# Performance work log

Hardware: AMD Instinct MI355X
Metric: run time of the kernel (lower is better)

Reference implementation:

```python
import jax, jax.numpy as jnp
import numpy as np

H = 8
D_MODEL = 1024
DIM_G = 64
WAVE_LEN = 1000.0


def box_relational_embedding(f_g):
    # f_g: [B, N, 4] -> [B, N, N, 64] trigonometric geometry embedding
    B, N, _ = f_g.shape
    x_min, y_min, x_max, y_max = jnp.split(f_g, 4, axis=-1)  # each [B, N, 1]
    cx = (x_min + x_max) * 0.5
    cy = (y_min + y_max) * 0.5
    w = x_max - x_min + 1.0
    h = y_max - y_min + 1.0
    # row i vs column j deltas, normalized by row box size
    dx = jnp.log(jnp.maximum(jnp.abs((cx - cx.reshape(B, 1, N)) / w), 1e-3))
    dy = jnp.log(jnp.maximum(jnp.abs((cy - cy.reshape(B, 1, N)) / h), 1e-3))
    dw = jnp.log(w / w.reshape(B, 1, N))
    dh = jnp.log(h / h.reshape(B, 1, N))
    pos = jnp.stack([dx, dy, dw, dh], axis=-1)  # [B, N, N, 4]
    feat_range = jnp.arange(DIM_G // 8, dtype=jnp.float32) / (DIM_G / 8.0)
    dim_mat = 1.0 / jnp.power(WAVE_LEN, feat_range)  # [8]
    mul = (100.0 * pos)[..., None] * dim_mat  # [B, N, N, 4, 8]
    mul = mul.reshape(B, N, N, DIM_G // 2)
    return jnp.concatenate([jnp.sin(mul), jnp.cos(mul)], axis=-1)  # [B, N, N, 64]


def setup_inputs() -> dict:
    key = jax.random.key(0)
    ks = jax.random.split(key, 12)
    B, N, D = 16, 256, D_MODEL
    q = jax.random.normal(ks[0], (B, N, D), jnp.float32)
    k = jax.random.normal(ks[1], (B, N, D), jnp.float32)
    v = jax.random.normal(ks[2], (B, N, D), jnp.float32)
    # valid boxes: x_max > x_min, y_max > y_min
    xy = jax.random.uniform(ks[3], (B, N, 2), jnp.float32) * 100.0
    wh = jax.random.uniform(ks[4], (B, N, 2), jnp.float32) * 50.0 + 1.0
    input_box = jnp.concatenate([xy, xy + wh], axis=-1)  # [B, N, 4]
    s = 0.02
    Wq = jax.random.normal(ks[5], (D, D), jnp.float32) * s
    Wk = jax.random.normal(ks[6], (D, D), jnp.float32) * s
    Wv = jax.random.normal(ks[7], (D, D), jnp.float32) * s
    Wo = jax.random.normal(ks[8], (D, D), jnp.float32) * s
    bq = jnp.zeros((D,), jnp.float32)
    bk = jnp.zeros((D,), jnp.float32)
    bv = jnp.zeros((D,), jnp.float32)
    bo = jnp.zeros((D,), jnp.float32)
    Wg = jax.random.normal(ks[9], (H, DIM_G), jnp.float32) * 0.1  # stacked per-head Linear(64,1)
    bg = jax.random.normal(ks[10], (H,), jnp.float32) * 0.1
    return {"input_query": q, "input_key": k, "input_value": v, "input_box": input_box,
            "Wq": Wq, "bq": bq, "Wk": Wk, "bk": bk, "Wv": Wv, "bv": bv,
            "Wg": Wg, "bg": bg, "Wo": Wo, "bo": bo}


def reference(input_query, input_key, input_value, input_box,
              Wq, bq, Wk, bk, Wv, bv, Wg, bg, Wo, bo):
    B, N, D = input_query.shape
    d_k = D // H

    def proj(x, W, b):
        return (x @ W + b).reshape(B, N, H, d_k).transpose(0, 2, 1, 3)  # [B,H,N,dk]

    q = proj(input_query, Wq, bq)
    k = proj(input_key, Wk, bk)
    v = proj(input_value, Wv, bv)

    emb = box_relational_embedding(input_box)  # [B, N, N, 64]
    # per-head Linear(64 -> 1), stacked: [B, H, N, N]
    rel_w = jax.nn.relu(jnp.einsum('bmng,hg->bhmn', emb, Wg) + bg[None, :, None, None])

    scores = jnp.einsum('bhqd,bhkd->bhqk', q, k) / np.sqrt(d_k).astype(np.float32)
    logits = jnp.log(jnp.maximum(rel_w, 1e-6)) + scores
    attn = jax.nn.softmax(logits, axis=-1)  # [B, H, N, N]
    out = jnp.einsum('bhqk,bhkd->bhqd', attn, v)
    out = out.transpose(0, 2, 1, 3).reshape(B, N, D)
    return out @ Wo + bo
```

## Files before the change

### kernel.cpp

```cpp
#include <hip/hip_runtime.h>
#include <hip/hip_bf16.h>
#include <hip/hip_fp16.h>
#include <math.h>

#define B_  16
#define N_  256
#define D_  1024
#define H_  8
#define DK_ 128

typedef unsigned short u16;
typedef __attribute__((ext_vector_type(8))) short s8v;
typedef __attribute__((ext_vector_type(4))) float f4v;

__device__ __forceinline__ u16 f2b(float x) {
    union { float f; unsigned u; } v; v.f = x;
    unsigned r = v.u + 0x7fffu + ((v.u >> 16) & 1u);
    return (u16)(r >> 16);
}

__device__ __forceinline__ void gload16(void* lds, const void* g) {
    __builtin_amdgcn_global_load_lds(
        (const __attribute__((address_space(1))) void*)g,
        (__attribute__((address_space(3))) void*)lds, 16, 0, 0);
}

#define WV_(n) asm volatile("s_waitcnt vmcnt(" #n ")" ::: "memory")
#define WV(n)  WV_(n)
#define MEMBAR() asm volatile("" ::: "memory")

__global__ __launch_bounds__(256)
void cvt_kernel(const float* __restrict__ x0, const float* __restrict__ x1,
                const float* __restrict__ x2, u16* __restrict__ out)
{
    const float* in = (blockIdx.y == 0) ? x0 : (blockIdx.y == 1) ? x1 : x2;
    u16* o = out + (size_t)blockIdx.y * 4194304;
    const int i = blockIdx.x * 256 + threadIdx.x;
    const float4 a = ((const float4*)in)[2 * i];
    const float4 b = ((const float4*)in)[2 * i + 1];
    union { u16 s[8]; uint4 v; } t;
    t.s[0] = f2b(a.x); t.s[1] = f2b(a.y); t.s[2] = f2b(a.z); t.s[3] = f2b(a.w);
    t.s[4] = f2b(b.x); t.s[5] = f2b(b.y); t.s[6] = f2b(b.z); t.s[7] = f2b(b.w);
    ((uint4*)o)[i] = t.v;
}

__global__ __launch_bounds__(256)
void cvtT_kernel(const float* __restrict__ W0, const float* __restrict__ W1,
                 const float* __restrict__ W2, const float* __restrict__ W3,
                 u16* __restrict__ out)
{
    const float* W = (blockIdx.z == 0) ? W0 : (blockIdx.z == 1) ? W1 :
                     (blockIdx.z == 2) ? W2 : W3;
    u16* o = out + (size_t)blockIdx.z * (D_ * D_);
    __shared__ float t[32][33];
    const int k0 = blockIdx.x * 32, n0 = blockIdx.y * 32;
    const int c = threadIdx.x & 31, r8 = threadIdx.x >> 5;
#pragma unroll
    for (int rr = 0; rr < 4; ++rr)
        t[r8 + rr * 8][c] = W[(size_t)(k0 + r8 + rr * 8) * D_ + n0 + c];
    __syncthreads();
#pragma unroll
    for (int rr = 0; rr < 4; ++rr)
        o[(size_t)(n0 + r8 + rr * 8) * D_ + k0 + c] = f2b(t[c][r8 + rr * 8]);
}

#define AOFF(s,mh) (((s)*2+(mh))*8192)
#define BOFF(s,nh) (32768 + ((s)*2+(nh))*8192)

#define STG_A(ns, mh, kn) do { \
    gload16(&lds8[AOFF(ns,mh) + adst],        aS + (size_t)(m0 + (mh)*64) * 1024 + (kn)); \
    gload16(&lds8[AOFF(ns,mh) + 4096 + adst], aS + (size_t)(m0 + 128 + (mh)*64) * 1024 + (kn)); \
} while (0)

#define STG_B(ns, nh, kn) do { \
    gload16(&lds8[BOFF(ns,nh) + bdst],        bS + (size_t)(n0 + (nh)*32) * 1024 + (kn)); \
    gload16(&lds8[BOFF(ns,nh) + 4096 + bdst], bS + (size_t)(n0 + 128 + (nh)*32) * 1024 + (kn)); \
} while (0)

#define TILE(S, W0, W1, W2, DOSTG, KN) do { \
     \
    WV(W0); __builtin_amdgcn_s_barrier(); \
    _Pragma("unroll") \
    for (int i = 0; i < 4; ++i) { \
        af[i][0] = *(const s8v*)&lds8[AOFF(S,0) + ar + i * 1024 + o0]; \
        af[i][1] = *(const s8v*)&lds8[AOFF(S,0) + ar + i * 1024 + o1]; } \
    _Pragma("unroll") \
    for (int j = 0; j < 2; ++j) { \
        bf0[j][0] = *(const s8v*)&lds8[BOFF(S,0) + br + j * 1024 + o0]; \
        bf0[j][1] = *(const s8v*)&lds8[BOFF(S,0) + br + j * 1024 + o1]; } \
    if (DOSTG) { STG_A((S)^1, 0, KN); STG_B((S)^1, 0, KN); } \
    __builtin_amdgcn_s_setprio(1); \
    _Pragma("unroll") \
    for (int i = 0; i < 4; ++i) \
        _Pragma("unroll") \
        for (int j = 0; j < 2; ++j) { \
            acc[i][j] = __builtin_amdgcn_mfma_f32_16x16x32_bf16(af[i][0], bf0[j][0], acc[i][j], 0, 0, 0); \
            acc[i][j] = __builtin_amdgcn_mfma_f32_16x16x32_bf16(af[i][1], bf0[j][1], acc[i][j], 0, 0, 0); } \
    __builtin_amdgcn_s_setprio(0); \
     \
    WV(W1); __builtin_amdgcn_s_barrier(); \
    _Pragma("unroll") \
    for (int j = 0; j < 2; ++j) { \
        bf1[j][0] = *(const s8v*)&lds8[BOFF(S,1) + br + j * 1024 + o0]; \
        bf1[j][1] = *(const s8v*)&lds8[BOFF(S,1) + br + j * 1024 + o1]; } \
    if (DOSTG) { STG_B((S)^1, 1, KN); } \
    __builtin_amdgcn_s_setprio(1); \
    _Pragma("unroll") \
    for (int i = 0; i < 4; ++i) \
        _Pragma("unroll") \
        for (int j = 0; j < 2; ++j) { \
            acc[i][2+j] = __builtin_amdgcn_mfma_f32_16x16x32_bf16(af[i][0], bf1[j][0], acc[i][2+j], 0, 0, 0); \
            acc[i][2+j] = __builtin_amdgcn_mfma_f32_16x16x32_bf16(af[i][1], bf1[j][1], acc[i][2+j], 0, 0, 0); } \
    __builtin_amdgcn_s_setprio(0); \
     \
    WV(W2); __builtin_amdgcn_s_barrier(); \
    _Pragma("unroll") \
    for (int i = 0; i < 4; ++i) { \
        af[i][0] = *(const s8v*)&lds8[AOFF(S,1) + ar + i * 1024 + o0]; \
        af[i][1] = *(const s8v*)&lds8[AOFF(S,1) + ar + i * 1024 + o1]; } \
    if (DOSTG) { STG_A((S)^1, 1, KN); } \
    __builtin_amdgcn_s_setprio(1); \
    _Pragma("unroll") \
    for (int i = 0; i < 4; ++i) \
        _Pragma("unroll") \
        for (int j = 0; j < 2; ++j) { \
            acc[4+i][2+j] = __builtin_amdgcn_mfma_f32_16x16x32_bf16(af[i][0], bf1[j][0], acc[4+i][2+j], 0, 0, 0); \
            acc[4+i][2+j] = __builtin_amdgcn_mfma_f32_16x16x32_bf16(af[i][1], bf1[j][1], acc[4+i][2+j], 0, 0, 0); } \
    __builtin_amdgcn_s_setprio(0); \
     \
    __builtin_amdgcn_s_setprio(1); \
    _Pragma("unroll") \
    for (int i = 0; i < 4; ++i) \
        _Pragma("unroll") \
        for (int j = 0; j < 2; ++j) { \
            acc[4+i][j] = __builtin_amdgcn_mfma_f32_16x16x32_bf16(af[i][0], bf0[j][0], acc[4+i][j], 0, 0, 0); \
            acc[4+i][j] = __builtin_amdgcn_mfma_f32_16x16x32_bf16(af[i][1], bf0[j][1], acc[4+i][j], 0, 0, 0); } \
    __builtin_amdgcn_s_setprio(0); \
} while (0)

template<int MODE>
__global__ __launch_bounds__(512, 2)
void gemm8(const u16* __restrict__ A0, const u16* __restrict__ Wt0,
           const float* __restrict__ b0, const float* __restrict__ b1,
           const float* __restrict__ b2, void* __restrict__ outb)
{
    extern __shared__ u16 lds8[];

    const int z = blockIdx.z;
    const u16* A  = A0  + (size_t)z * 4194304;
    const u16* Wt = Wt0 + (size_t)z * 1048576;
    const float* bias = (z == 0) ? b0 : (z == 1) ? b1 : b2;

    const int bid = blockIdx.x;
    const int m0  = (bid & 15) * 256;
    const int n0  = (bid >> 4) * 256;

    const int tid  = threadIdx.x;
    const int lane = tid & 63;
    const int w    = tid >> 6;
    const int l15  = lane & 15;
    const int l4   = lane >> 4;
    const int wr   = w >> 2;
    const int wc   = w & 3;

    const int ar = wr * 4096 + l15 * 64;
    const int br = wc * 2048 + l15 * 64;
    const int o0 = (l4 ^ (l15 & 7)) * 8;
    const int o1 = o0 ^ 32;

    const int rA   = tid >> 3;
    const int cswz = ((tid & 7) ^ (rA & 7)) * 8;
    const u16* aS  = A  + (size_t)rA * 1024 + cswz;
    const u16* bS  = Wt + (size_t)((tid >> 8) * 64 + (rA & 31)) * 1024 + cswz;
    const int adst = rA * 64 + (tid & 7) * 8;
    const int bdst = (tid >> 8) * 2048 + (rA & 31) * 64 + (tid & 7) * 8;

    f4v acc[8][4] = {};
    s8v af[4][2], bf0[2][2], bf1[2][2];

    STG_A(0, 0, 0); STG_B(0, 0, 0); MEMBAR();
    STG_B(0, 1, 0); MEMBAR();
    STG_A(0, 1, 0); MEMBAR();

#pragma unroll 1
    for (int tt = 0; tt < 14; tt += 2) {
        TILE(0, 4, 6, 6, true, (tt + 1) * 64);
        TILE(1, 4, 6, 6, true, (tt + 2) * 64);
    }
    TILE(0, 4, 6, 6, true, 15 * 64);
    TILE(1, 4, 2, 0, false, 0);

#pragma unroll
    for (int mh = 0; mh < 2; ++mh)
#pragma unroll
    for (int i = 0; i < 4; ++i)
#pragma unroll
    for (int nh = 0; nh < 2; ++nh)
#pragma unroll
    for (int j = 0; j < 2; ++j) {
        const int n = n0 + wc * 64 + nh * 32 + j * 16 + l15;
        const float bb = bias[n];
        const int mbase = m0 + wr * 128 + mh * 64 + i * 16 + l4 * 4;
        const f4v a = acc[mh * 4 + i][nh * 2 + j];
        if constexpr (MODE == 0) {
#pragma unroll
            for (int reg = 0; reg < 4; ++reg)
                ((float*)outb)[(size_t)(mbase + reg) * 1024 + n] = a[reg] + bb;
        } else {
            if (z == 2) {
                const int b = mbase >> 8, tok = mbase & 255;
                const int h = n >> 7, d = n & 127;
                ushort4 st;
                st.x = f2b(a[0] + bb); st.y = f2b(a[1] + bb);
                st.z = f2b(a[2] + bb); st.w = f2b(a[3] + bb);
                *(ushort4*)&((u16*)outb)[(size_t)z * 4194304 +
                    (((size_t)b * H_ + h) * DK_ + d) * N_ + tok] = st;
            } else {
                const int h = n >> 7, d = n & 127;
#pragma unroll
                for (int reg = 0; reg < 4; ++reg) {
                    const int m = mbase + reg;
                    const int b = m >> 8, tok = m & 255;
                    ((u16*)outb)[(size_t)z * 4194304 +
                        (((size_t)b * H_ + h) * N_ + tok) * DK_ + d] = f2b(a[reg] + bb);
                }
            }
        }
    }
}

__global__ __launch_bounds__(256)
void boxbias_kernel(const float* __restrict__ fg, const float* __restrict__ Wg,
                    const float* __restrict__ bg, _Float16* __restrict__ lb)
{
    __shared__ float sWg[512];
    __shared__ float sbg[8];
    const int tid = threadIdx.x;
    const int b = blockIdx.x >> 8;
    const int i = blockIdx.x & 255;

    sWg[tid] = Wg[tid];
    sWg[tid + 256] = Wg[tid + 256];
    if (tid < 8) sbg[tid] = bg[tid];

    const float4 bi = *(const float4*)&fg[(size_t)(b * N_ + i) * 4];
    const float cxi = 0.5f * (bi.x + bi.z);
    const float cyi = 0.5f * (bi.y + bi.w);
    const float wi  = bi.z - bi.x + 1.0f;
    const float hi  = bi.w - bi.y + 1.0f;

    const int j = tid;
    const float4 bj = *(const float4*)&fg[(size_t)(b * N_ + j) * 4];
    const float cxj = 0.5f * (bj.x + bj.z);
    const float cyj = 0.5f * (bj.y + bj.w);
    const float wj  = bj.z - bj.x + 1.0f;
    const float hj  = bj.w - bj.y + 1.0f;

    const float pos[4] = {
        logf(fmaxf(fabsf((cxi - cxj) / wi), 1e-3f)) * 100.0f,
        logf(fmaxf(fabsf((cyi - cyj) / hi), 1e-3f)) * 100.0f,
        logf(wi / wj) * 100.0f,
        logf(hi / hj) * 100.0f
    };
    const float dim[8] = {1.0f, 0.421696503f, 0.177827941f, 0.0749894209f,
                          0.0316227766f, 0.0133352143f, 0.00562341325f, 0.00237137371f};

    float sv[32], cv[32];
#pragma unroll
    for (int p = 0; p < 4; ++p)
#pragma unroll
        for (int q = 0; q < 8; ++q)
            __sincosf(pos[p] * dim[q], &sv[p * 8 + q], &cv[p * 8 + q]);

    __syncthreads();
#pragma unroll
    for (int h = 0; h < 8; ++h) {
        float acc = sbg[h];
        const float* wrow = &sWg[h * 64];
#pragma unroll
        for (int g = 0; g < 32; ++g)
            acc = fmaf(sv[g], wrow[g], fmaf(cv[g], wrow[32 + g], acc));
        const float rel = fmaxf(acc, 0.0f);
        lb[(((size_t)b * H_ + h) * N_ + i) * N_ + j] =
            (_Float16)logf(fmaxf(rel, 1e-6f));
    }
}

__global__ __launch_bounds__(256)
void attn_mfma_kernel(const u16* __restrict__ qp, const u16* __restrict__ kp,
                      const u16* __restrict__ vp, const _Float16* __restrict__ lb,
                      u16* __restrict__ ao)
{
    __shared__ __align__(16) u16 Ks[32][136];
    __shared__ __align__(16) u16 Vt[128][40];
    __shared__ __align__(16) u16 Ps[4][32][40];

    const int tid  = threadIdx.x;
    const int lane = tid & 63;
    const int w    = tid >> 6;
    const int l15  = lane & 15;
    const int l4   = lane >> 4;
    const int bh   = blockIdx.x >> 1;
    const int qt   = blockIdx.x & 1;
    const int q0   = qt * 128 + w * 32;

    s8v qf[2][4];
    const u16* qb = qp + ((size_t)bh * N_ + q0) * DK_;
#pragma unroll
    for (int mf = 0; mf < 2; ++mf)
#pragma unroll
        for (int ks = 0; ks < 4; ++ks)
            qf[mf][ks] = *(const s8v*)(qb + (size_t)(mf * 16 + l15) * DK_ + ks * 32 + l4 * 8);

    f4v o[2][8] = {};
    float m_r[2][4], l_r[2][4];
#pragma unroll
    for (int mf = 0; mf < 2; ++mf)
#pragma unroll
        for (int r = 0; r < 4; ++r) { m_r[mf][r] = -INFINITY; l_r[mf][r] = 0.0f; }

    const float scale = 0.08838834764831845f;
    const _Float16* lbb = lb + ((size_t)bh * N_ + q0) * N_;

    const int sr = tid >> 3;
    const int sc = (tid & 7) * 16;
    const int vr = tid >> 2;
    const int vs = (tid & 3) * 8;

    for (int kt = 0; kt < 8; ++kt) {
        __syncthreads();
        {
            const u16* ksrc = kp + ((size_t)bh * N_ + kt * 32) * DK_;
            *(s8v*)&Ks[sr][sc]     = *(const s8v*)(ksrc + (size_t)sr * DK_ + sc);
            *(s8v*)&Ks[sr][sc + 8] = *(const s8v*)(ksrc + (size_t)sr * DK_ + sc + 8);
        }
        {
            const u16* vsrc = vp + ((size_t)bh * DK_ + vr) * N_ + kt * 32 + vs;
            const s8v v0 = *(const s8v*)vsrc;
            const s8v v1 = *(const s8v*)(vsrc + 64 * N_);
            *(s8v*)&Vt[vr][vs]      = v0;
            *(s8v*)&Vt[vr + 64][vs] = v1;
        }
        __syncthreads();

        f4v s[2][2] = {};
#pragma unroll
        for (int ks = 0; ks < 4; ++ks) {
#pragma unroll
            for (int kf = 0; kf < 2; ++kf) {
                const s8v kb = *(const s8v*)&Ks[kf * 16 + l15][ks * 32 + l4 * 8];
#pragma unroll
                for (int mf = 0; mf < 2; ++mf)
                    s[mf][kf] = __builtin_amdgcn_mfma_f32_16x16x32_bf16(
                        qf[mf][ks], kb, s[mf][kf], 0, 0, 0);
            }
        }
#pragma unroll
        for (int mf = 0; mf < 2; ++mf)
#pragma unroll
            for (int kf = 0; kf < 2; ++kf)
#pragma unroll
                for (int r = 0; r < 4; ++r)
                    s[mf][kf][r] = fmaf(s[mf][kf][r], scale, (float)
                        lbb[(size_t)(mf * 16 + l4 * 4 + r) * N_ + kt * 32 + kf * 16 + l15]);

#pragma unroll
        for (int mf = 0; mf < 2; ++mf) {
            float rm[4], al[4];
#pragma unroll
            for (int r = 0; r < 4; ++r) rm[r] = fmaxf(s[mf][0][r], s[mf][1][r]);
#pragma unroll
            for (int st = 1; st <= 8; st <<= 1)
#pragma unroll
                for (int r = 0; r < 4; ++r) rm[r] = fmaxf(rm[r], __shfl_xor(rm[r], st));
#pragma unroll
            for (int r = 0; r < 4; ++r) {
                const float mn = fmaxf(m_r[mf][r], rm[r]);
                al[r] = __expf(m_r[mf][r] - mn);
                m_r[mf][r] = mn;
            }
            float p0[4], p1[4], rs[4];
#pragma unroll
            for (int r = 0; r < 4; ++r) {
                p0[r] = __expf(s[mf][0][r] - m_r[mf][r]);
                p1[r] = __expf(s[mf][1][r] - m_r[mf][r]);
                rs[r] = p0[r] + p1[r];
            }
#pragma unroll
            for (int st = 1; st <= 8; st <<= 1)
#pragma unroll
                for (int r = 0; r < 4; ++r) rs[r] += __shfl_xor(rs[r], st);
#pragma unroll
            for (int r = 0; r < 4; ++r) {
                l_r[mf][r] = l_r[mf][r] * al[r] + rs[r];
                Ps[w][mf * 16 + l4 * 4 + r][l15]      = f2b(p0[r]);
                Ps[w][mf * 16 + l4 * 4 + r][16 + l15] = f2b(p1[r]);
            }
#pragma unroll
            for (int nf = 0; nf < 8; ++nf)
#pragma unroll
                for (int r = 0; r < 4; ++r) o[mf][nf][r] *= al[r];
        }

        s8v pa[2];
#pragma unroll
        for (int mf = 0; mf < 2; ++mf)
            pa[mf] = *(const s8v*)&Ps[w][mf * 16 + l15][l4 * 8];
#pragma unroll
        for (int nf = 0; nf < 8; ++nf) {
            const s8v vb = *(const s8v*)&Vt[nf * 16 + l15][l4 * 8];
#pragma unroll
            for (int mf = 0; mf < 2; ++mf)
                o[mf][nf] = __builtin_amdgcn_mfma_f32_16x16x32_bf16(
                    pa[mf], vb, o[mf][nf], 0, 0, 0);
        }
    }

    const int b = bh >> 3, h = bh & 7;
#pragma unroll
    for (int mf = 0; mf < 2; ++mf) {
        float inv[4];
#pragma unroll
        for (int r = 0; r < 4; ++r) inv[r] = 1.0f / l_r[mf][r];
#pragma unroll
        for (int nf = 0; nf < 8; ++nf) {
#pragma unroll
            for (int r = 0; r < 4; ++r) {
                const int tok = q0 + mf * 16 + l4 * 4 + r;
                const int d = nf * 16 + l15;
                ao[(((size_t)b * N_ + tok) * H_ + h) * DK_ + d] = f2b(o[mf][nf][r] * inv[r]);
            }
        }
    }
}

extern "C" void kernel_launch(void* const* d_in, const int* in_sizes, int n_in,
                              void* d_out, int out_size, void* d_ws, size_t ws_size,
                              hipStream_t stream)
{
    const float* xq = (const float*)d_in[0];
    const float* xk = (const float*)d_in[1];
    const float* xv = (const float*)d_in[2];
    const float* fg = (const float*)d_in[3];
    const float* Wq = (const float*)d_in[4];
    const float* bq = (const float*)d_in[5];
    const float* Wk = (const float*)d_in[6];
    const float* bk = (const float*)d_in[7];
    const float* Wv = (const float*)d_in[8];
    const float* bv = (const float*)d_in[9];
    const float* Wg = (const float*)d_in[10];
    const float* bg = (const float*)d_in[11];
    const float* Wo = (const float*)d_in[12];
    const float* bo = (const float*)d_in[13];

    char* w8 = (char*)d_ws;
    u16*      xb  = (u16*)(w8);
    u16*      Wt  = (u16*)(w8 + 25165824);
    u16*      qkv = (u16*)(w8 + 33554432);
    _Float16* lb  = (_Float16*)(w8 + 58720256);
    u16*      ao  = (u16*)(w8 + 75497472);

    (void)hipFuncSetAttribute(reinterpret_cast<const void*>(&gemm8<1>),
                              hipFuncAttributeMaxDynamicSharedMemorySize, 131072);
    (void)hipFuncSetAttribute(reinterpret_cast<const void*>(&gemm8<0>),
                              hipFuncAttributeMaxDynamicSharedMemorySize, 131072);

    cvt_kernel<<<dim3(2048, 3), 256, 0, stream>>>(xq, xk, xv, xb);
    cvtT_kernel<<<dim3(32, 32, 4), 256, 0, stream>>>(Wq, Wk, Wv, Wo, Wt);

    gemm8<1><<<dim3(64, 1, 3), 512, 131072, stream>>>(xb, Wt, bq, bk, bv, qkv);

    boxbias_kernel<<<B_ * N_, 256, 0, stream>>>(fg, Wg, bg, lb);

    attn_mfma_kernel<<<B_ * H_ * 2, 256, 0, stream>>>(
        qkv, qkv + 4194304, qkv + 2 * 4194304, lb, ao);

    gemm8<0><<<dim3(64, 1, 1), 512, 131072, stream>>>(
        ao, Wt + 3 * 1048576, bo, bo, bo, d_out);
}
```

Baseline: 133.7 us.

## Restructure GEMM tile pipeline, remap blocks, and split attention into more blocks

The GEMM main loop is rebuilt into 8-phase tiles. Each phase issues its next-stage global-to-LDS loads before a barrier and adds a second barrier after its MFMA group, and one B-fragment register set replaces two. Block index to M-tile mapping is swizzled so neighbouring blocks share weight columns. The attention kernel now gives each wave 16 query rows instead of 32 and launches twice as many blocks, for more parallelism across CUs. In exchange, K/V tiles are loaded into LDS twice as many times in total, and the extra barriers may add stalls.

Result: no change. 134.4 us (+0.5%).

```diff
diff --git a/kernel.cpp b/kernel.cpp
--- a/kernel.cpp
+++ b/kernel.cpp
@@ -28,6 +28,7 @@
 #define WV_(n) asm volatile("s_waitcnt vmcnt(" #n ")" ::: "memory")
 #define WV(n)  WV_(n)
 #define MEMBAR() asm volatile("" ::: "memory")
+#define BAR() __builtin_amdgcn_s_barrier()
 
 __global__ __launch_bounds__(256)
 void cvt_kernel(const float* __restrict__ x0, const float* __restrict__ x1,
@@ -77,65 +78,60 @@
     gload16(&lds8[BOFF(ns,nh) + 4096 + bdst], bS + (size_t)(n0 + 128 + (nh)*32) * 1024 + (kn)); \
 } while (0)
 
-#define TILE(S, W0, W1, W2, DOSTG, KN) do { \
-     \
-    WV(W0); __builtin_amdgcn_s_barrier(); \
+#define RD_A(S, mh) do { \
     _Pragma("unroll") \
     for (int i = 0; i < 4; ++i) { \
-        af[i][0] = *(const s8v*)&lds8[AOFF(S,0) + ar + i * 1024 + o0]; \
-        af[i][1] = *(const s8v*)&lds8[AOFF(S,0) + ar + i * 1024 + o1]; } \
+        af[i][0] = *(const s8v*)&lds8[AOFF(S,mh) + ar + i * 1024 + o0]; \
+        af[i][1] = *(const s8v*)&lds8[AOFF(S,mh) + ar + i * 1024 + o1]; } \
+} while (0)
+
+#define RD_B(S, nh) do { \
     _Pragma("unroll") \
     for (int j = 0; j < 2; ++j) { \
-        bf0[j][0] = *(const s8v*)&lds8[BOFF(S,0) + br + j * 1024 + o0]; \
-        bf0[j][1] = *(const s8v*)&lds8[BOFF(S,0) + br + j * 1024 + o1]; } \
-    if (DOSTG) { STG_A((S)^1, 0, KN); STG_B((S)^1, 0, KN); } \
+        bf[j][0] = *(const s8v*)&lds8[BOFF(S,nh) + br + j * 1024 + o0]; \
+        bf[j][1] = *(const s8v*)&lds8[BOFF(S,nh) + br + j * 1024 + o1]; } \
+} while (0)
+
+#define MM(i0, j0) do { \
     __builtin_amdgcn_s_setprio(1); \
     _Pragma("unroll") \
     for (int i = 0; i < 4; ++i) \
         _Pragma("unroll") \
         for (int j = 0; j < 2; ++j) { \
-            acc[i][j] = __builtin_amdgcn_mfma_f32_16x16x32_bf16(af[i][0], bf0[j][0], acc[i][j], 0, 0, 0); \
-            acc[i][j] = __builtin_amdgcn_mfma_f32_16x16x32_bf16(af[i][1], bf0[j][1], acc[i][j], 0, 0, 0); } \
+            acc[(i0)+i][(j0)+j] = __builtin_amdgcn_mfma_f32_16x16x32_bf16( \
+                af[i][0], bf[j][0], acc[(i0)+i][(j0)+j], 0, 0, 0); \
+            acc[(i0)+i][(j0)+j] = __builtin_amdgcn_mfma_f32_16x16x32_bf16( \
+                af[i][1], bf[j][1], acc[(i0)+i][(j0)+j], 0, 0, 0); } \
     __builtin_amdgcn_s_setprio(0); \
+} while (0)
+
+#define TILE8(S, KN, DOSTG, W1, W2) do { \
      \
-    WV(W1); __builtin_amdgcn_s_barrier(); \
-    _Pragma("unroll") \
-    for (int j = 0; j < 2; ++j) { \
-        bf1[j][0] = *(const s8v*)&lds8[BOFF(S,1) + br + j * 1024 + o0]; \
-        bf1[j][1] = *(const s8v*)&lds8[BOFF(S,1) + br + j * 1024 + o1]; } \
+    WV(4); \
+    if (DOSTG) { STG_A((S)^1, 0, KN); } \
+    BAR(); \
+    RD_A(S, 0); RD_B(S, 0); \
+    MM(0, 0); \
+    BAR(); \
+     \
+    WV(W1); \
+    if (DOSTG) { STG_B((S)^1, 0, KN); } \
+    BAR(); \
+    RD_B(S, 1); \
+    MM(0, 2); \
+    BAR(); \
+     \
+    WV(W2); \
     if (DOSTG) { STG_B((S)^1, 1, KN); } \
-    __builtin_amdgcn_s_setprio(1); \
-    _Pragma("unroll") \
-    for (int i = 0; i < 4; ++i) \
-        _Pragma("unroll") \
-        for (int j = 0; j < 2; ++j) { \
-            acc[i][2+j] = __builtin_amdgcn_mfma_f32_16x16x32_bf16(af[i][0], bf1[j][0], acc[i][2+j], 0, 0, 0); \
-            acc[i][2+j] = __builtin_amdgcn_mfma_f32_16x16x32_bf16(af[i][1], bf1[j][1], acc[i][2+j], 0, 0, 0); } \
-    __builtin_amdgcn_s_setprio(0); \
+    BAR(); \
+    RD_A(S, 1); \
+    MM(4, 2); \
+    BAR(); \
      \
-    WV(W2); __builtin_amdgcn_s_barrier(); \
-    _Pragma("unroll") \
-    for (int i = 0; i < 4; ++i) { \
-        af[i][0] = *(const s8v*)&lds8[AOFF(S,1) + ar + i * 1024 + o0]; \
-        af[i][1] = *(const s8v*)&lds8[AOFF(S,1) + ar + i * 1024 + o1]; } \
     if (DOSTG) { STG_A((S)^1, 1, KN); } \
-    __builtin_amdgcn_s_setprio(1); \
-    _Pragma("unroll") \
-    for (int i = 0; i < 4; ++i) \
-        _Pragma("unroll") \
-        for (int j = 0; j < 2; ++j) { \
-            acc[4+i][2+j] = __builtin_amdgcn_mfma_f32_16x16x32_bf16(af[i][0], bf1[j][0], acc[4+i][2+j], 0, 0, 0); \
-            acc[4+i][2+j] = __builtin_amdgcn_mfma_f32_16x16x32_bf16(af[i][1], bf1[j][1], acc[4+i][2+j], 0, 0, 0); } \
-    __builtin_amdgcn_s_setprio(0); \
-     \
-    __builtin_amdgcn_s_setprio(1); \
-    _Pragma("unroll") \
-    for (int i = 0; i < 4; ++i) \
-        _Pragma("unroll") \
-        for (int j = 0; j < 2; ++j) { \
-            acc[4+i][j] = __builtin_amdgcn_mfma_f32_16x16x32_bf16(af[i][0], bf0[j][0], acc[4+i][j], 0, 0, 0); \
-            acc[4+i][j] = __builtin_amdgcn_mfma_f32_16x16x32_bf16(af[i][1], bf0[j][1], acc[4+i][j], 0, 0, 0); } \
-    __builtin_amdgcn_s_setprio(0); \
+    RD_B(S, 0); \
+    MM(4, 0); \
+    BAR(); \
 } while (0)
 
 template<int MODE>
@@ -152,8 +148,10 @@
     const float* bias = (z == 0) ? b0 : (z == 1) ? b1 : b2;
 
     const int bid = blockIdx.x;
-    const int m0  = (bid & 15) * 256;
-    const int n0  = (bid >> 4) * 256;
+    const int by  = (bid & 7) * 2 + ((bid >> 3) & 1);
+    const int bx  = bid >> 4;
+    const int m0  = by * 256;
+    const int n0  = bx * 256;
 
     const int tid  = threadIdx.x;
     const int lane = tid & 63;
@@ -176,19 +174,20 @@
     const int bdst = (tid >> 8) * 2048 + (rA & 31) * 64 + (tid & 7) * 8;
 
     f4v acc[8][4] = {};
-    s8v af[4][2], bf0[2][2], bf1[2][2];
-
-    STG_A(0, 0, 0); STG_B(0, 0, 0); MEMBAR();
+    s8v af[4][2], bf[2][2];
+
+    STG_A(0, 0, 0); MEMBAR();
+    STG_B(0, 0, 0); MEMBAR();
     STG_B(0, 1, 0); MEMBAR();
     STG_A(0, 1, 0); MEMBAR();
 
 #pragma unroll 1
-    for (int tt = 0; tt < 14; tt += 2) {
-        TILE(0, 4, 6, 6, true, (tt + 1) * 64);
-        TILE(1, 4, 6, 6, true, (tt + 2) * 64);
+    for (int tt = 0; tt < 7; ++tt) {
+        TILE8(0, (2 * tt + 1) * 64, 1, 4, 4);
+        TILE8(1, (2 * tt + 2) * 64, 1, 4, 4);
     }
-    TILE(0, 4, 6, 6, true, 15 * 64);
-    TILE(1, 4, 2, 0, false, 0);
+    TILE8(0, 960, 1, 4, 4);
+    TILE8(1, 0, 0, 2, 0);
 
 #pragma unroll
     for (int mh = 0; mh < 2; ++mh)
@@ -293,31 +292,27 @@
 {
     __shared__ __align__(16) u16 Ks[32][136];
     __shared__ __align__(16) u16 Vt[128][40];
-    __shared__ __align__(16) u16 Ps[4][32][40];
+    __shared__ __align__(16) u16 Ps[4][16][40];
 
     const int tid  = threadIdx.x;
     const int lane = tid & 63;
     const int w    = tid >> 6;
     const int l15  = lane & 15;
     const int l4   = lane >> 4;
-    const int bh   = blockIdx.x >> 1;
-    const int qt   = blockIdx.x & 1;
-    const int q0   = qt * 128 + w * 32;
-
-    s8v qf[2][4];
+    const int bh   = blockIdx.x >> 2;
+    const int qt   = blockIdx.x & 3;
+    const int q0   = qt * 64 + w * 16;
+
+    s8v qf[4];
     const u16* qb = qp + ((size_t)bh * N_ + q0) * DK_;
 #pragma unroll
-    for (int mf = 0; mf < 2; ++mf)
-#pragma unroll
-        for (int ks = 0; ks < 4; ++ks)
-            qf[mf][ks] = *(const s8v*)(qb + (size_t)(mf * 16 + l15) * DK_ + ks * 32 + l4 * 8);
-
-    f4v o[2][8] = {};
-    float m_r[2][4], l_r[2][4];
-#pragma unroll
-    for (int mf = 0; mf < 2; ++mf)
-#pragma unroll
-        for (int r = 0; r < 4; ++r) { m_r[mf][r] = -INFINITY; l_r[mf][r] = 0.0f; }
+    for (int ks = 0; ks < 4; ++ks)
+        qf[ks] = *(const s8v*)(qb + (size_t)l15 * DK_ + ks * 32 + l4 * 8);
+
+    f4v o[8] = {};
+    float m_r[4], l_r[4];
+#pragma unroll
+    for (int r = 0; r < 4; ++r) { m_r[r] = -INFINITY; l_r[r] = 0.0f; }
 
     const float scale = 0.08838834764831845f;
     const _Float16* lbb = lb + ((size_t)bh * N_ + q0) * N_;
@@ -343,47 +338,42 @@
         }
         __syncthreads();
 
-        f4v s[2][2] = {};
+        f4v s[2] = {};
 #pragma unroll
         for (int ks = 0; ks < 4; ++ks) {
 #pragma unroll
             for (int kf = 0; kf < 2; ++kf) {
                 const s8v kb = *(const s8v*)&Ks[kf * 16 + l15][ks * 32 + l4 * 8];
-#pragma unroll
-                for (int mf = 0; mf < 2; ++mf)
-                    s[mf][kf] = __builtin_amdgcn_mfma_f32_16x16x32_bf16(
-                        qf[mf][ks], kb, s[mf][kf], 0, 0, 0);
+                s[kf] = __builtin_amdgcn_mfma_f32_16x16x32_bf16(
+                    qf[ks], kb, s[kf], 0, 0, 0);
             }
         }
 #pragma unroll
-        for (int mf = 0; mf < 2; ++mf)
-#pragma unroll
-            for (int kf = 0; kf < 2; ++kf)
-#pragma unroll
-                for (int r = 0; r < 4; ++r)
-                    s[mf][kf][r] = fmaf(s[mf][kf][r], scale, (float)
-                        lbb[(size_t)(mf * 16 + l4 * 4 + r) * N_ + kt * 32 + kf * 16 + l15]);
-
-#pragma unroll
-        for (int mf = 0; mf < 2; ++mf) {
+        for (int kf = 0; kf < 2; ++kf)
+#pragma unroll
+            for (int r = 0; r < 4; ++r)
+                s[kf][r] = fmaf(s[kf][r], scale, (float)
+                    lbb[(size_t)(l4 * 4 + r) * N_ + kt * 32 + kf * 16 + l15]);
+
+        {
             float rm[4], al[4];
 #pragma unroll
-            for (int r = 0; r < 4; ++r) rm[r] = fmaxf(s[mf][0][r], s[mf][1][r]);
+            for (int r = 0; r < 4; ++r) rm[r] = fmaxf(s[0][r], s[1][r]);
 #pragma unroll
             for (int st = 1; st <= 8; st <<= 1)
 #pragma unroll
                 for (int r = 0; r < 4; ++r) rm[r] = fmaxf(rm[r], __shfl_xor(rm[r], st));
 #pragma unroll
             for (int r = 0; r < 4; ++r) {
-                const float mn = fmaxf(m_r[mf][r], rm[r]);
-                al[r] = __expf(m_r[mf][r] - mn);
-                m_r[mf][r] = mn;
+                const float mn = fmaxf(m_r[r], rm[r]);
+                al[r] = __expf(m_r[r] - mn);
+                m_r[r] = mn;
             }
             float p0[4], p1[4], rs[4];
 #pragma unroll
             for (int r = 0; r < 4; ++r) {
-                p0[r] = __expf(s[mf][0][r] - m_r[mf][r]);
-                p1[r] = __expf(s[mf][1][r] - m_r[mf][r]);
+                p0[r] = __expf(s[0][r] - m_r[r]);
+                p1[r] = __expf(s[1][r] - m_r[r]);
                 rs[r] = p0[r] + p1[r];
             }
 #pragma unroll
@@ -392,44 +382,35 @@
                 for (int r = 0; r < 4; ++r) rs[r] += __shfl_xor(rs[r], st);
 #pragma unroll
             for (int r = 0; r < 4; ++r) {
-                l_r[mf][r] = l_r[mf][r] * al[r] + rs[r];
-                Ps[w][mf * 16 + l4 * 4 + r][l15]      = f2b(p0[r]);
-                Ps[w][mf * 16 + l4 * 4 + r][16 + l15] = f2b(p1[r]);
+                l_r[r] = l_r[r] * al[r] + rs[r];
+                Ps[w][l4 * 4 + r][l15]      = f2b(p0[r]);
+                Ps[w][l4 * 4 + r][16 + l15] = f2b(p1[r]);
             }
 #pragma unroll
             for (int nf = 0; nf < 8; ++nf)
 #pragma unroll
-                for (int r = 0; r < 4; ++r) o[mf][nf][r] *= al[r];
-        }
-
-        s8v pa[2];
-#pragma unroll
-        for (int mf = 0; mf < 2; ++mf)
-            pa[mf] = *(const s8v*)&Ps[w][mf * 16 + l15][l4 * 8];
+                for (int r = 0; r < 4; ++r) o[nf][r] *= al[r];
+        }
+
+        const s8v pa = *(const s8v*)&Ps[w][l15][l4 * 8];
 #pragma unroll
         for (int nf = 0; nf < 8; ++nf) {
             const s8v vb = *(const s8v*)&Vt[nf * 16 + l15][l4 * 8];
-#pragma unroll
-            for (int mf = 0; mf < 2; ++mf)
-                o[mf][nf] = __builtin_amdgcn_mfma_f32_16x16x32_bf16(
-                    pa[mf], vb, o[mf][nf], 0, 0, 0);
+            o[nf] = __builtin_amdgcn_mfma_f32_16x16x32_bf16(pa, vb, o[nf], 0, 0, 0);
         }
     }
 
     const int b = bh >> 3, h = bh & 7;
-#pragma unroll
-    for (int mf = 0; mf < 2; ++mf) {
-        float inv[4];
-#pragma unroll
-        for (int r = 0; r < 4; ++r) inv[r] = 1.0f / l_r[mf][r];
-#pragma unroll
-        for (int nf = 0; nf < 8; ++nf) {
-#pragma unroll
-            for (int r = 0; r < 4; ++r) {
-                const int tok = q0 + mf * 16 + l4 * 4 + r;
-                const int d = nf * 16 + l15;
-                ao[(((size_t)b * N_ + tok) * H_ + h) * DK_ + d] = f2b(o[mf][nf][r] * inv[r]);
-            }
+    float inv[4];
+#pragma unroll
+    for (int r = 0; r < 4; ++r) inv[r] = 1.0f / l_r[r];
+#pragma unroll
+    for (int nf = 0; nf < 8; ++nf) {
+#pragma unroll
+        for (int r = 0; r < 4; ++r) {
+            const int tok = q0 + l4 * 4 + r;
+            const int d = nf * 16 + l15;
+            ao[(((size_t)b * N_ + tok) * H_ + h) * DK_ + d] = f2b(o[nf][r] * inv[r]);
         }
     }
 }
@@ -472,7 +453,7 @@
 
     boxbias_kernel<<<B_ * N_, 256, 0, stream>>>(fg, Wg, bg, lb);
 
-    attn_mfma_kernel<<<B_ * H_ * 2, 256, 0, stream>>>(
+    attn_mfma_kernel<<<B_ * H_ * 4, 256, 0, stream>>>(
         qkv, qkv + 4194304, qkv + 2 * 4194304, lb, ao);
 
     gemm8<0><<<dim3(64, 1, 1), 512, 131072, stream>>>(
```
